# Kernel optimization log

Measured on AMD Instinct MI355X. Metric: run time of the kernel, lower is better.

The kernel has to match this reference:

```python
import jax, jax.numpy as jnp
import numpy as np

B, S, E, H = 2, 2048, 1024, 16
D = E // H  # head_dim = 64
EPS = 1e-6


def _angle_decay():
    # angle: 1/10000**linspace(0,1,D//2), each value repeated twice (interleaved)
    a = 1.0 / (10000.0 ** jnp.linspace(0.0, 1.0, D // 2))
    angle = jnp.repeat(a, 2)  # [D]
    decay = jnp.log(1.0 - 2.0 ** (-5.0 - jnp.arange(H, dtype=jnp.float32)))  # [H]
    return angle, decay


def _rel_pos(slen):
    angle, decay = _angle_decay()
    idx = jnp.arange(slen, dtype=jnp.float32)
    sin = jnp.sin(idx[:, None] * angle[None, :])  # [S, D]
    cos = jnp.cos(idx[:, None] * angle[None, :])  # [S, D]
    diff = idx[:, None] - idx[None, :]            # [S, S]
    tril = diff >= 0
    masked = jnp.where(tril, diff, jnp.inf)
    mask = jnp.exp(masked * decay[:, None, None])  # [H, S, S]; exp(-inf)=0 on upper tri
    mask = jnp.nan_to_num(mask)
    mask = mask / jnp.sqrt(jnp.sum(mask, axis=-1, keepdims=True))
    return sin, cos, mask


def _rotate_every_two(x):
    x1 = x[..., ::2]
    x2 = x[..., 1::2]
    return jnp.stack((-x2, x1), axis=-1).reshape(x.shape)


def _theta_shift(x, sin, cos):
    # x: [B, H, S, D]; sin/cos: [S, D] broadcast over B,H
    return x * cos + _rotate_every_two(x) * sin


def setup_inputs() -> dict:
    key = jax.random.key(0)
    ks = jax.random.split(key, 5)
    scale = 1.0 / np.sqrt(E)
    return {
        "x": jax.random.normal(ks[0], (B, S, E), dtype=jnp.float32),
        "Wq": jax.random.normal(ks[1], (E, E), dtype=jnp.float32) * scale,
        "Wk": jax.random.normal(ks[2], (E, E), dtype=jnp.float32) * scale,
        "Wv": jax.random.normal(ks[3], (E, E), dtype=jnp.float32) * scale,
        "Wg": jax.random.normal(ks[4], (E, E), dtype=jnp.float32) * scale,
    }


def reference(x, Wq, Wk, Wv, Wg):
    bsz, tgt_len, _ = x.shape
    sin, cos, mask = _rel_pos(tgt_len)
    scaling = E ** (-0.5)

    q = x @ Wq
    k = (x @ Wk) * scaling
    v = x @ Wv
    g = x @ Wg

    q = q.reshape(bsz, tgt_len, H, D).transpose(0, 2, 1, 3)  # [B,H,S,D]
    k = k.reshape(bsz, tgt_len, H, D).transpose(0, 2, 1, 3)
    vr = v.reshape(bsz, tgt_len, H, D).transpose(0, 2, 1, 3)

    qr = _theta_shift(q, sin, cos)
    kr = _theta_shift(k, sin, cos)

    qk = jnp.einsum("bhqd,bhkd->bhqk", qr, kr) * mask[None]
    denom = jax.lax.stop_gradient(
        jnp.clip(jnp.sum(jnp.abs(qk), axis=-1, keepdims=True), 1.0, 5e4)
    )
    out = jnp.einsum("bhqk,bhkd->bhqd", qk / denom, vr)
    out = out.transpose(0, 2, 1, 3)  # [B,S,H,D]

    # RMSNorm over head_dim (no affine)
    out = out * jax.lax.rsqrt(jnp.mean(out * out, axis=-1, keepdims=True) + EPS)
    out = out.reshape(bsz, tgt_len, E)
    return jax.nn.silu(g) * out
```

## Files before the change

kernel.cpp:

```cpp
#include <hip/hip_runtime.h>

typedef unsigned short u16;
typedef unsigned int u32;
typedef __attribute__((ext_vector_type(8))) __bf16 bf16x8;
typedef __attribute__((ext_vector_type(4))) float f32x4;

#define B_SZ   2
#define S_LEN  2048
#define E_DIM  1024
#define NHEAD  16
#define HD     64
#define KDIM   1024
#define NOUT   4096

__device__ __forceinline__ float bf2f(u16 u){
  union { u32 i; float f; } c; c.i = ((u32)u) << 16; return c.f;
}
__device__ __forceinline__ u16 f2bf(float f){
  union { float f; u32 i; } c; c.f = f;
  return (u16)((c.i + 0x7FFFu + ((c.i >> 16) & 1u)) >> 16);
}
__device__ __forceinline__ u16 f2bf_fast(float f){
  union { float f; u32 i; } c; c.f = f;
  return (u16)((c.i + 0x8000u) >> 16);
}
__device__ __forceinline__ void gl2lds16(const void* g, void* l){
  __builtin_amdgcn_global_load_lds((const __attribute__((address_space(1))) void*)g,
                                   (__attribute__((address_space(3))) void*)l, 16, 0, 0);
}

__global__ __launch_bounds__(256) void castx_kernel(const float* __restrict__ x, u16* __restrict__ xb){
  size_t flat = ((size_t)blockIdx.x * 256 + threadIdx.x) * 16;
  int m7 = (int)((flat >> 10) & 7);
  int cb = (int)((flat >> 3) & 7);
  size_t tile = flat & ~(size_t)63;
  float f[16];
  #pragma unroll
  for (int c = 0; c < 4; c++) *(float4*)&f[c * 4] = *(const float4*)&x[flat + c * 4];
  u16 o[16];
  #pragma unroll
  for (int i = 0; i < 16; i++) o[i] = f2bf(f[i]);
  *(uint4*)&xb[tile + ((cb ^ m7) * 8)]       = *(uint4*)&o[0];
  *(uint4*)&xb[tile + (((cb + 1) ^ m7) * 8)] = *(uint4*)&o[8];
}

__global__ __launch_bounds__(256) void wtrans_kernel(const float* __restrict__ Wq, const float* __restrict__ Wk,
                                                     const float* __restrict__ Wv, const float* __restrict__ Wg,
                                                     u16* __restrict__ WT){
  const float* Ws[4] = {Wq, Wk, Wv, Wg};
  const float* W = Ws[blockIdx.z];
  int n0 = blockIdx.x * 64, k0 = blockIdx.y * 64;
  __shared__ u16 tile[64][66];
  int t = threadIdx.x;
  int r = t >> 2, cg = (t & 3) * 16;
  const float* src = W + (size_t)(k0 + r) * E_DIM + n0 + cg;
  float f[16];
  #pragma unroll
  for (int c = 0; c < 4; c++) *(float4*)&f[c * 4] = *(const float4*)&src[c * 4];
  #pragma unroll
  for (int i = 0; i < 16; i++) tile[r][cg + i] = f2bf(f[i]);
  __syncthreads();
  u16 ov[16];
  #pragma unroll
  for (int i = 0; i < 16; i++) ov[i] = tile[cg + i][r];
  int n7 = r & 7, cb = cg >> 3;
  u16* dst = WT + (size_t)(blockIdx.z * E_DIM + n0 + r) * KDIM + k0;
  *(uint4*)&dst[(cb ^ n7) * 8]       = *(uint4*)&ov[0];
  *(uint4*)&dst[((cb + 1) ^ n7) * 8] = *(uint4*)&ov[8];
}

__global__ __launch_bounds__(256) void gemm_kernel(const u16* __restrict__ A, const u16* __restrict__ Bt,
                                                   u16* __restrict__ C){
  __shared__ __align__(16) u16 As[128 * 64];
  __shared__ __align__(16) u16 Bs[128 * 64];
  int m0 = blockIdx.y * 128, n0 = blockIdx.x * 128;
  int t = threadIdx.x;
  int wave = t >> 6, lane = t & 63;
  int l15 = lane & 15, quad = lane >> 4, h8 = lane & 7;
  int r0 = (wave & 1) * 64, c0 = (wave >> 1) * 64;
  f32x4 acc[4][4];
  #pragma unroll
  for (int i = 0; i < 4; i++)
    #pragma unroll
    for (int j = 0; j < 4; j++) acc[i][j] = (f32x4){0.f, 0.f, 0.f, 0.f};

  for (int k0 = 0; k0 < KDIM; k0 += 64){
    __syncthreads();
    #pragma unroll
    for (int c = 0; c < 4; c++){
      int L = c * 256 + t;
      gl2lds16(A + (size_t)(m0 + (L >> 3)) * KDIM + k0 + (L & 7) * 8, &As[L * 8]);
    }
    #pragma unroll
    for (int c = 0; c < 4; c++){
      int L = c * 256 + t;
      gl2lds16(Bt + (size_t)(n0 + (L >> 3)) * KDIM + k0 + (L & 7) * 8, &Bs[L * 8]);
    }
    __syncthreads();
    #pragma unroll
    for (int kk = 0; kk < 2; kk++){
      bf16x8 a[4], b[4];
      #pragma unroll
      for (int i = 0; i < 4; i++) a[i] = *(const bf16x8*)&As[(r0 + i * 16 + l15) * 64 + ((kk * 4 + quad) ^ h8) * 8];
      #pragma unroll
      for (int j = 0; j < 4; j++) b[j] = *(const bf16x8*)&Bs[(c0 + j * 16 + l15) * 64 + ((kk * 4 + quad) ^ h8) * 8];
      #pragma unroll
      for (int i = 0; i < 4; i++)
        #pragma unroll
        for (int j = 0; j < 4; j++)
          acc[i][j] = __builtin_amdgcn_mfma_f32_16x16x32_bf16(a[i], b[j], acc[i][j], 0, 0, 0);
    }
  }
  #pragma unroll
  for (int i = 0; i < 4; i++){
    int row = m0 + r0 + i * 16 + quad * 4;
    #pragma unroll
    for (int j = 0; j < 4; j++){
      int col = n0 + c0 + j * 16 + l15;
      #pragma unroll
      for (int r = 0; r < 4; r++)
        C[(size_t)(row + r) * NOUT + col] = f2bf(acc[i][j][r]);
    }
  }
}

__global__ __launch_bounds__(256) void shift_kernel(const u16* __restrict__ qkvg,
                                                    u16* __restrict__ qr, u16* __restrict__ kr,
                                                    u16* __restrict__ vt, u16* __restrict__ gc){
  int sb = blockIdx.x, bh = blockIdx.y;
  int s0 = sb * 64;
  int t = threadIdx.x;
  int sl = t >> 2, dg = (t & 3) * 16;
  int s = s0 + sl;
  int h = bh & 15;
  size_t token = (size_t)(bh >> 4) * S_LEN + s;
  size_t base = token * NOUT + h * HD + dg;
  u16 qv[16], kv[16], vv[16], gv[16];
  *(uint4*)&qv[0] = *(const uint4*)&qkvg[base];
  *(uint4*)&qv[8] = *(const uint4*)&qkvg[base + 8];
  *(uint4*)&kv[0] = *(const uint4*)&qkvg[base + 1024];
  *(uint4*)&kv[8] = *(const uint4*)&qkvg[base + 1024 + 8];
  *(uint4*)&vv[0] = *(const uint4*)&qkvg[base + 2048];
  *(uint4*)&vv[8] = *(const uint4*)&qkvg[base + 2048 + 8];
  *(uint4*)&gv[0] = *(const uint4*)&qkvg[base + 3072];
  *(uint4*)&gv[8] = *(const uint4*)&qkvg[base + 3072 + 8];
  size_t gdst = token * E_DIM + h * HD + dg;
  *(uint4*)&gc[gdst]     = *(uint4*)&gv[0];
  *(uint4*)&gc[gdst + 8] = *(uint4*)&gv[8];
  u16 qo[16], ko[16];
  #pragma unroll
  for (int i = 0; i < 8; i++){
    int dd = dg + 2 * i;
    float a = exp2f(-(float)(dd >> 1) * (13.287712379549449f / 31.0f));
    float ang = (float)s * a;
    float sn = sinf(ang), cs = cosf(ang);
    float qe = bf2f(qv[2 * i]), qd = bf2f(qv[2 * i + 1]);
    qo[2 * i]     = f2bf(qe * cs - qd * sn);
    qo[2 * i + 1] = f2bf(qd * cs + qe * sn);
    float ke = bf2f(kv[2 * i]) * 0.03125f, kd = bf2f(kv[2 * i + 1]) * 0.03125f;
    ko[2 * i]     = f2bf(ke * cs - kd * sn);
    ko[2 * i + 1] = f2bf(kd * cs + ke * sn);
  }
  size_t dsto = ((size_t)bh * S_LEN + s) * HD;
  *(uint4*)&qr[dsto + dg]     = *(uint4*)&qo[0];
  *(uint4*)&qr[dsto + dg + 8] = *(uint4*)&qo[8];
  int s7 = s & 7, cbk = dg >> 3;
  *(uint4*)&kr[dsto + ((cbk ^ s7) * 8)]       = *(uint4*)&ko[0];
  *(uint4*)&kr[dsto + (((cbk + 1) ^ s7) * 8)] = *(uint4*)&ko[8];
  __shared__ u16 vs[64][66];
  #pragma unroll
  for (int i = 0; i < 16; i++) vs[sl][dg + i] = vv[i];
  __syncthreads();
  int d = t >> 2, jg = (t & 3) * 16;
  u16 ov[16];
  #pragma unroll
  for (int i = 0; i < 16; i++) ov[i] = vs[jg + i][d];
  int d7 = d & 7, cbv = jg >> 3;
  size_t vrow = ((size_t)bh * HD + d) * S_LEN + s0;
  *(uint4*)&vt[vrow + ((cbv ^ d7) * 8)]       = *(uint4*)&ov[0];
  *(uint4*)&vt[vrow + (((cbv + 1) ^ d7) * 8)] = *(uint4*)&ov[8];
}

__global__ __launch_bounds__(256, 2) void retention_kernel(const u16* __restrict__ qr, const u16* __restrict__ kr,
                                                           const u16* __restrict__ vt,
                                                           float* __restrict__ pO, float* __restrict__ pBa){
  int bh = blockIdx.x;
  int qb = 15 - (int)blockIdx.y;
  int z  = blockIdx.z;
  int h = bh & 15;
  int q0 = qb * 128;
  __shared__ __align__(16) u16 Ks[64 * 64];
  __shared__ __align__(16) u16 Vs[64 * 64];
  __shared__ __align__(16) u16 Ps[128 * 72];
  int t = threadIdx.x, wave = t >> 6, lane = t & 63;
  int l15 = lane & 15, quad = lane >> 4, h8 = lane & 7;

  float decay = log1pf(-exp2f(-5.0f - (float)h));
  float negd = -decay;
  float estep = __expf(64.0f * negd);

  int qsE[2], rowb[2];
  #pragma unroll
  for (int e = 0; e < 2; e++){ rowb[e] = wave * 32 + e * 16; qsE[e] = q0 + rowb[e]; }

  bf16x8 qB[2][2];
  #pragma unroll
  for (int e = 0; e < 2; e++){
    size_t qrow = ((size_t)bh * S_LEN + qsE[e] + l15) * HD;
    qB[e][0] = *(const bf16x8*)&qr[qrow + quad * 8];
    qB[e][1] = *(const bf16x8*)&qr[qrow + 32 + quad * 8];
  }

  float win_f = 18.0f / negd;
  int win_i = (win_f > 2.1e9f) ? 0x7f000000 : (int)win_f;
  int z_lo = z ? (qb + 1) : 0;
  int z_hi = z ? (2 * qb + 1) : qb;
  int kb_lo = z_lo;
  {
    int jmin = q0 - win_i;
    if (jmin > z_lo * 64){ int wlo = jmin >> 6; kb_lo = wlo > z_lo ? wlo : z_lo; }
  }
  int k0s = kb_lo * 64;

  float em1d = expm1f(decay);
  float rfE[2]; int iE[2];
  #pragma unroll
  for (int e = 0; e < 2; e++){
    int i = qsE[e] + l15;
    iE[e] = i;
    float rowsum = expm1f((float)(i + 1) * decay) / em1d;
    rfE[e] = __expf((float)(i - k0s) * decay) * rsqrtf(rowsum);
  }
  float e1 = __expf(negd);
  float c16 = __expf(negd * 16.0f);
  float cbr[4];
  cbr[0] = __expf(negd * (float)(quad * 4));
  cbr[1] = cbr[0] * e1; cbr[2] = cbr[1] * e1; cbr[3] = cbr[2] * e1;

  f32x4 o[2][4];
  #pragma unroll
  for (int e = 0; e < 2; e++)
    #pragma unroll
    for (int dt = 0; dt < 4; dt++) o[e][dt] = (f32x4){0.f, 0.f, 0.f, 0.f};
  float babs[2] = {0.f, 0.f};

  const u16* krbh = kr + (size_t)bh * S_LEN * HD;
  const u16* vtbh = vt + (size_t)bh * HD * S_LEN;

  for (int kb = kb_lo; kb <= z_hi; kb++){
    int k0 = kb * 64;
    __syncthreads();
    #pragma unroll
    for (int c = 0; c < 2; c++){
      int L = c * 256 + t;
      gl2lds16(krbh + (size_t)k0 * HD + L * 8, &Ks[L * 8]);
    }
    #pragma unroll
    for (int c = 0; c < 2; c++){
      int L = c * 256 + t;
      gl2lds16(vtbh + (size_t)(L >> 3) * S_LEN + k0 + (L & 7) * 8, &Vs[L * 8]);
    }
    __syncthreads();

    bf16x8 kA0[4], kA1[4];
    #pragma unroll
    for (int ct = 0; ct < 4; ct++){
      int rw = (ct * 16 + l15) * 64;
      kA0[ct] = *(const bf16x8*)&Ks[rw + ((quad ^ h8) * 8)];
      kA1[ct] = *(const bf16x8*)&Ks[rw + (((quad + 4) ^ h8) * 8)];
    }
    #pragma unroll
    for (int e = 0; e < 2; e++){
      int qs = qsE[e];
      if (k0 <= qs + 15 && k0 + 63 >= qs - win_i){
        bool diag = (k0 + 64 > qs);
        float cf[4] = {cbr[0], cbr[1], cbr[2], cbr[3]};
        #pragma unroll
        for (int ct = 0; ct < 4; ct++){
          f32x4 zacc = (f32x4){0.f, 0.f, 0.f, 0.f};
          zacc = __builtin_amdgcn_mfma_f32_16x16x32_bf16(kA0[ct], qB[e][0], zacc, 0, 0, 0);
          zacc = __builtin_amdgcn_mfma_f32_16x16x32_bf16(kA1[ct], qB[e][1], zacc, 0, 0, 0);
          u16 pk[4];
          #pragma unroll
          for (int r = 0; r < 4; r++){
            float p = zacc[r] * (rfE[e] * cf[r]);
            if (diag && (k0 + ct * 16 + quad * 4 + r) > iE[e]) p = 0.f;
            babs[e] += fabsf(p);
            pk[r] = f2bf_fast(p);
            cf[r] *= c16;
          }
          u32 lo = (u32)pk[0] | ((u32)pk[1] << 16);
          u32 hi = (u32)pk[2] | ((u32)pk[3] << 16);
          *(uint2*)&Ps[(rowb[e] + l15) * 72 + ct * 16 + quad * 4] = make_uint2(lo, hi);
        }
      }
    }
    #pragma unroll
    for (int e = 0; e < 2; e++){
      int qs = qsE[e];
      if (k0 <= qs + 15 && k0 + 63 >= qs - win_i){
        bf16x8 pB0 = *(const bf16x8*)&Ps[(rowb[e] + l15) * 72 + quad * 8];
        bf16x8 pB1 = *(const bf16x8*)&Ps[(rowb[e] + l15) * 72 + 32 + quad * 8];
        #pragma unroll
        for (int dt = 0; dt < 4; dt++){
          int rw = (dt * 16 + l15) * 64;
          bf16x8 vA0 = *(const bf16x8*)&Vs[rw + ((quad ^ h8) * 8)];
          bf16x8 vA1 = *(const bf16x8*)&Vs[rw + (((quad + 4) ^ h8) * 8)];
          o[e][dt] = __builtin_amdgcn_mfma_f32_16x16x32_bf16(vA0, pB0, o[e][dt], 0, 0, 0);
          o[e][dt] = __builtin_amdgcn_mfma_f32_16x16x32_bf16(vA1, pB1, o[e][dt], 0, 0, 0);
        }
      }
    }
    #pragma unroll
    for (int e = 0; e < 2; e++) rfE[e] *= estep;
  }

  size_t slot = ((size_t)bh * 16 + qb) * 2 + z;
  float* po = pO + slot * (4 * 128 * 16);
  #pragma unroll
  for (int e = 0; e < 2; e++){
    float bsum = babs[e];
    bsum += __shfl_xor(bsum, 16);
    bsum += __shfl_xor(bsum, 32);
    if (quad == 0) pBa[slot * 128 + rowb[e] + l15] = bsum;
    #pragma unroll
    for (int dt = 0; dt < 4; dt++)
      *(float4*)&po[(dt * 128 + rowb[e] + l15) * 16 + quad * 4] = *(float4*)&o[e][dt];
  }
}

__global__ __launch_bounds__(128) void combine_kernel(const float* __restrict__ pO, const float* __restrict__ pBa,
                                                      const u16* __restrict__ gc, float* __restrict__ out){
  int bh = blockIdx.x, qb = blockIdx.y;
  int b = bh >> 4, h = bh & 15;
  int i = threadIdx.x;
  int s = qb * 128 + i;
  size_t s2 = ((size_t)bh * 16 + qb) * 2;
  const float* p0 = pO + s2 * 8192;
  const float* p1 = p0 + 8192;
  float v[64];
  #pragma unroll
  for (int dt = 0; dt < 4; dt++)
    #pragma unroll
    for (int c = 0; c < 4; c++){
      float4 a  = *(const float4*)&p0[(dt * 128 + i) * 16 + c * 4];
      float4 bb = *(const float4*)&p1[(dt * 128 + i) * 16 + c * 4];
      int d = dt * 16 + c * 4;
      v[d + 0] = a.x + bb.x; v[d + 1] = a.y + bb.y;
      v[d + 2] = a.z + bb.z; v[d + 3] = a.w + bb.w;
    }
  float bsum = pBa[s2 * 128 + i] + pBa[(s2 + 1) * 128 + i];
  float dinv = 1.0f / fminf(fmaxf(bsum, 1.0f), 50000.0f);
  float ssq = 0.f;
  #pragma unroll
  for (int d = 0; d < 64; d++){ v[d] *= dinv; ssq += v[d] * v[d]; }
  float rms = rsqrtf(ssq * (1.0f / 64.0f) + 1e-6f);
  size_t gbase = ((size_t)b * S_LEN + s) * E_DIM + h * HD;
  u16 gu[64];
  #pragma unroll
  for (int c = 0; c < 8; c++) *(uint4*)&gu[c * 8] = *(const uint4*)&gc[gbase + c * 8];
  float ov[64];
  #pragma unroll
  for (int d = 0; d < 64; d++){
    float gv = bf2f(gu[d]);
    float sg = gv / (1.0f + __expf(-gv));
    ov[d] = v[d] * rms * sg;
  }
  float* obase = out + ((size_t)b * S_LEN + s) * E_DIM + h * HD;
  #pragma unroll
  for (int c = 0; c < 16; c++) *(float4*)&obase[c * 4] = *(float4*)&ov[c * 4];
}

extern "C" void kernel_launch(void* const* d_in, const int* in_sizes, int n_in,
                              void* d_out, int out_size, void* d_ws, size_t ws_size,
                              hipStream_t stream){
  const float* x  = (const float*)d_in[0];
  const float* Wq = (const float*)d_in[1];
  const float* Wk = (const float*)d_in[2];
  const float* Wv = (const float*)d_in[3];
  const float* Wg = (const float*)d_in[4];
  float* out = (float*)d_out;
  char* ws = (char*)d_ws;
  u16*   xb   = (u16*)(ws);
  u16*   WT   = (u16*)(ws + (8ull  << 20));
  u16*   qkvg = (u16*)(ws + (16ull << 20));
  u16*   qrp  = (u16*)(ws);
  u16*   vtp  = (u16*)(ws + (8ull  << 20));
  float* pO   = (float*)(ws + (16ull << 20));
  u16*   krp  = (u16*)(ws + (48ull << 20));
  u16*   gcp  = (u16*)(ws + (56ull << 20));
  float* pBa  = (float*)(ws + (64ull << 20));

  castx_kernel    <<<dim3(1024),       256, 0, stream>>>(x, xb);
  wtrans_kernel   <<<dim3(16, 16, 4),  256, 0, stream>>>(Wq, Wk, Wv, Wg, WT);
  gemm_kernel     <<<dim3(32, 32),     256, 0, stream>>>(xb, WT, qkvg);
  shift_kernel    <<<dim3(32, 32),     256, 0, stream>>>(qkvg, qrp, krp, vtp, gcp);
  retention_kernel<<<dim3(32, 16, 2),  256, 0, stream>>>(qrp, krp, vtp, pO, pBa);
  combine_kernel  <<<dim3(32, 16),     128, 0, stream>>>(pO, pBa, gcp, out);
}
```

Before: 195.1 us.

## Fuse rotary shift, V transpose and gate copy into GEMM epilogue

```diff
diff --git a/kernel.cpp b/kernel.cpp
--- a/kernel.cpp
+++ b/kernel.cpp
@@ -70,9 +70,11 @@
 }
 
 __global__ __launch_bounds__(256) void gemm_kernel(const u16* __restrict__ A, const u16* __restrict__ Bt,
-                                                   u16* __restrict__ C){
-  __shared__ __align__(16) u16 As[128 * 64];
-  __shared__ __align__(16) u16 Bs[128 * 64];
+                                                   u16* __restrict__ qr, u16* __restrict__ kr,
+                                                   u16* __restrict__ vt, u16* __restrict__ gc){
+  __shared__ __align__(16) u16 smem[17408];
+  u16* As = smem;
+  u16* Bs = smem + 8192;
   int m0 = blockIdx.y * 128, n0 = blockIdx.x * 128;
   int t = threadIdx.x;
   int wave = t >> 6, lane = t & 63;
@@ -111,74 +113,84 @@
           acc[i][j] = __builtin_amdgcn_mfma_f32_16x16x32_bf16(a[i], b[j], acc[i][j], 0, 0, 0);
     }
   }
-  #pragma unroll
-  for (int i = 0; i < 4; i++){
-    int row = m0 + r0 + i * 16 + quad * 4;
+
+  int zone = n0 >> 10;
+  int b = m0 >> 11;
+  int sbase = (m0 & 2047) + r0;
+
+  if (zone == 3){
+    int ebase = (n0 & 1023) + c0;
+    #pragma unroll
+    for (int i = 0; i < 4; i++){
+      int tok = m0 + r0 + i * 16 + quad * 4;
+      #pragma unroll
+      for (int j = 0; j < 4; j++){
+        int e = ebase + j * 16 + l15;
+        #pragma unroll
+        for (int r = 0; r < 4; r++)
+          gc[(size_t)(tok + r) * E_DIM + e] = f2bf(acc[i][j][r]);
+      }
+    }
+  } else if (zone == 2){
+    __syncthreads();
+    u16* Tw = smem + wave * 4352;
+    #pragma unroll
+    for (int i = 0; i < 4; i++)
+      #pragma unroll
+      for (int j = 0; j < 4; j++){
+        int d = j * 16 + l15;
+        u16 pk[4];
+        #pragma unroll
+        for (int r = 0; r < 4; r++) pk[r] = f2bf(acc[i][j][r]);
+        *(uint2*)&Tw[d * 68 + i * 16 + quad * 4] = *(uint2*)pk;
+      }
+    __syncthreads();
+    int h = ((n0 & 1023) >> 6) + (c0 >> 6);
+    size_t bh = (size_t)b * 16 + h;
+    int sgq = lane >> 4;
+    #pragma unroll
+    for (int it = 0; it < 4; it++){
+      int dd = (lane & 15) + 16 * it;
+      u16 ov[16];
+      *(uint4*)&ov[0] = *(const uint4*)&Tw[dd * 68 + sgq * 16];
+      *(uint4*)&ov[8] = *(const uint4*)&Tw[dd * 68 + sgq * 16 + 8];
+      int s0 = sbase + sgq * 16;
+      int d7 = dd & 7;
+      int cb = (s0 & 63) >> 3;
+      size_t vrow = (bh * HD + dd) * S_LEN + (s0 & ~63);
+      *(uint4*)&vt[vrow + ((cb ^ d7) * 8)]       = *(uint4*)&ov[0];
+      *(uint4*)&vt[vrow + (((cb + 1) ^ d7) * 8)] = *(uint4*)&ov[8];
+    }
+  } else {
+    float scale = (zone == 1) ? 0.03125f : 1.0f;
+    int h = ((n0 & 1023) >> 6) + (c0 >> 6);
+    size_t bh = (size_t)b * 16 + h;
+    float sgn = (l15 & 1) ? 1.0f : -1.0f;
     #pragma unroll
     for (int j = 0; j < 4; j++){
-      int col = n0 + c0 + j * 16 + l15;
-      #pragma unroll
-      for (int r = 0; r < 4; r++)
-        C[(size_t)(row + r) * NOUT + col] = f2bf(acc[i][j][r]);
-    }
-  }
-}
-
-__global__ __launch_bounds__(256) void shift_kernel(const u16* __restrict__ qkvg,
-                                                    u16* __restrict__ qr, u16* __restrict__ kr,
-                                                    u16* __restrict__ vt, u16* __restrict__ gc){
-  int sb = blockIdx.x, bh = blockIdx.y;
-  int s0 = sb * 64;
-  int t = threadIdx.x;
-  int sl = t >> 2, dg = (t & 3) * 16;
-  int s = s0 + sl;
-  int h = bh & 15;
-  size_t token = (size_t)(bh >> 4) * S_LEN + s;
-  size_t base = token * NOUT + h * HD + dg;
-  u16 qv[16], kv[16], vv[16], gv[16];
-  *(uint4*)&qv[0] = *(const uint4*)&qkvg[base];
-  *(uint4*)&qv[8] = *(const uint4*)&qkvg[base + 8];
-  *(uint4*)&kv[0] = *(const uint4*)&qkvg[base + 1024];
-  *(uint4*)&kv[8] = *(const uint4*)&qkvg[base + 1024 + 8];
-  *(uint4*)&vv[0] = *(const uint4*)&qkvg[base + 2048];
-  *(uint4*)&vv[8] = *(const uint4*)&qkvg[base + 2048 + 8];
-  *(uint4*)&gv[0] = *(const uint4*)&qkvg[base + 3072];
-  *(uint4*)&gv[8] = *(const uint4*)&qkvg[base + 3072 + 8];
-  size_t gdst = token * E_DIM + h * HD + dg;
-  *(uint4*)&gc[gdst]     = *(uint4*)&gv[0];
-  *(uint4*)&gc[gdst + 8] = *(uint4*)&gv[8];
-  u16 qo[16], ko[16];
-  #pragma unroll
-  for (int i = 0; i < 8; i++){
-    int dd = dg + 2 * i;
-    float a = exp2f(-(float)(dd >> 1) * (13.287712379549449f / 31.0f));
-    float ang = (float)s * a;
-    float sn = sinf(ang), cs = cosf(ang);
-    float qe = bf2f(qv[2 * i]), qd = bf2f(qv[2 * i + 1]);
-    qo[2 * i]     = f2bf(qe * cs - qd * sn);
-    qo[2 * i + 1] = f2bf(qd * cs + qe * sn);
-    float ke = bf2f(kv[2 * i]) * 0.03125f, kd = bf2f(kv[2 * i + 1]) * 0.03125f;
-    ko[2 * i]     = f2bf(ke * cs - kd * sn);
-    ko[2 * i + 1] = f2bf(kd * cs + ke * sn);
-  }
-  size_t dsto = ((size_t)bh * S_LEN + s) * HD;
-  *(uint4*)&qr[dsto + dg]     = *(uint4*)&qo[0];
-  *(uint4*)&qr[dsto + dg + 8] = *(uint4*)&qo[8];
-  int s7 = s & 7, cbk = dg >> 3;
-  *(uint4*)&kr[dsto + ((cbk ^ s7) * 8)]       = *(uint4*)&ko[0];
-  *(uint4*)&kr[dsto + (((cbk + 1) ^ s7) * 8)] = *(uint4*)&ko[8];
-  __shared__ u16 vs[64][66];
-  #pragma unroll
-  for (int i = 0; i < 16; i++) vs[sl][dg + i] = vv[i];
-  __syncthreads();
-  int d = t >> 2, jg = (t & 3) * 16;
-  u16 ov[16];
-  #pragma unroll
-  for (int i = 0; i < 16; i++) ov[i] = vs[jg + i][d];
-  int d7 = d & 7, cbv = jg >> 3;
-  size_t vrow = ((size_t)bh * HD + d) * S_LEN + s0;
-  *(uint4*)&vt[vrow + ((cbv ^ d7) * 8)]       = *(uint4*)&ov[0];
-  *(uint4*)&vt[vrow + (((cbv + 1) ^ d7) * 8)] = *(uint4*)&ov[8];
+      int d = j * 16 + l15;
+      float a = exp2f(-(float)(d >> 1) * (13.287712379549449f / 31.0f));
+      #pragma unroll
+      for (int i = 0; i < 4; i++){
+        #pragma unroll
+        for (int r = 0; r < 4; r++){
+          int s = sbase + i * 16 + quad * 4 + r;
+          float v = acc[i][j][r] * scale;
+          float p = __shfl_xor(v, 1);
+          float ang = (float)s * a;
+          float sn = __sinf(ang), cs = __cosf(ang);
+          float rv = fmaf(sgn * p, sn, v * cs);
+          size_t base = (bh * S_LEN + s) * HD;
+          if (zone == 0){
+            qr[base + d] = f2bf(rv);
+          } else {
+            int cb = d >> 3, s7 = s & 7;
+            kr[base + ((cb ^ s7) * 8) + (d & 7)] = f2bf(rv);
+          }
+        }
+      }
+    }
+  }
 }
 
 __global__ __launch_bounds__(256, 2) void retention_kernel(const u16* __restrict__ qr, const u16* __restrict__ kr,
@@ -381,20 +393,18 @@
   const float* Wg = (const float*)d_in[4];
   float* out = (float*)d_out;
   char* ws = (char*)d_ws;
-  u16*   xb   = (u16*)(ws);
-  u16*   WT   = (u16*)(ws + (8ull  << 20));
-  u16*   qkvg = (u16*)(ws + (16ull << 20));
-  u16*   qrp  = (u16*)(ws);
-  u16*   vtp  = (u16*)(ws + (8ull  << 20));
-  float* pO   = (float*)(ws + (16ull << 20));
-  u16*   krp  = (u16*)(ws + (48ull << 20));
-  u16*   gcp  = (u16*)(ws + (56ull << 20));
-  float* pBa  = (float*)(ws + (64ull << 20));
+  u16*   xb  = (u16*)(ws);
+  u16*   WT  = (u16*)(ws + (8ull  << 20));
+  float* pO  = (float*)(ws);
+  u16*   qrp = (u16*)(ws + (32ull << 20));
+  u16*   krp = (u16*)(ws + (40ull << 20));
+  u16*   vtp = (u16*)(ws + (48ull << 20));
+  u16*   gcp = (u16*)(ws + (56ull << 20));
+  float* pBa = (float*)(ws + (64ull << 20));
 
   castx_kernel    <<<dim3(1024),       256, 0, stream>>>(x, xb);
   wtrans_kernel   <<<dim3(16, 16, 4),  256, 0, stream>>>(Wq, Wk, Wv, Wg, WT);
-  gemm_kernel     <<<dim3(32, 32),     256, 0, stream>>>(xb, WT, qkvg);
-  shift_kernel    <<<dim3(32, 32),     256, 0, stream>>>(qkvg, qrp, krp, vtp, gcp);
+  gemm_kernel     <<<dim3(32, 32),     256, 0, stream>>>(xb, WT, qrp, krp, vtp, gcp);
   retention_kernel<<<dim3(32, 16, 2),  256, 0, stream>>>(qrp, krp, vtp, pO, pBa);
   combine_kernel  <<<dim3(32, 16),     128, 0, stream>>>(pO, pBa, gcp, out);
 }
```

Result: slower. 232.5 us (+19.2%).

## Write gate directly from GEMM, store partial outputs in bf16, shrink decay window

Applied to the files above, without the earlier changes.

```diff
diff --git a/kernel.cpp b/kernel.cpp
--- a/kernel.cpp
+++ b/kernel.cpp
@@ -11,7 +11,7 @@
 #define NHEAD  16
 #define HD     64
 #define KDIM   1024
-#define NOUT   4096
+#define NQKV   3072
 
 __device__ __forceinline__ float bf2f(u16 u){
   union { u32 i; float f; } c; c.i = ((u32)u) << 16; return c.f;
@@ -70,7 +70,7 @@
 }
 
 __global__ __launch_bounds__(256) void gemm_kernel(const u16* __restrict__ A, const u16* __restrict__ Bt,
-                                                   u16* __restrict__ C){
+                                                   u16* __restrict__ qkv, u16* __restrict__ gc){
   __shared__ __align__(16) u16 As[128 * 64];
   __shared__ __align__(16) u16 Bs[128 * 64];
   int m0 = blockIdx.y * 128, n0 = blockIdx.x * 128;
@@ -111,22 +111,36 @@
           acc[i][j] = __builtin_amdgcn_mfma_f32_16x16x32_bf16(a[i], b[j], acc[i][j], 0, 0, 0);
     }
   }
-  #pragma unroll
-  for (int i = 0; i < 4; i++){
-    int row = m0 + r0 + i * 16 + quad * 4;
-    #pragma unroll
-    for (int j = 0; j < 4; j++){
-      int col = n0 + c0 + j * 16 + l15;
-      #pragma unroll
-      for (int r = 0; r < 4; r++)
-        C[(size_t)(row + r) * NOUT + col] = f2bf(acc[i][j][r]);
-    }
-  }
-}
-
-__global__ __launch_bounds__(256) void shift_kernel(const u16* __restrict__ qkvg,
+  if (n0 < 3072){
+    #pragma unroll
+    for (int i = 0; i < 4; i++){
+      int row = m0 + r0 + i * 16 + quad * 4;
+      #pragma unroll
+      for (int j = 0; j < 4; j++){
+        int col = n0 + c0 + j * 16 + l15;
+        #pragma unroll
+        for (int r = 0; r < 4; r++)
+          qkv[(size_t)(row + r) * NQKV + col] = f2bf(acc[i][j][r]);
+      }
+    }
+  } else {
+    #pragma unroll
+    for (int i = 0; i < 4; i++){
+      int row = m0 + r0 + i * 16 + quad * 4;
+      #pragma unroll
+      for (int j = 0; j < 4; j++){
+        int e = (n0 - 3072) + c0 + j * 16 + l15;
+        #pragma unroll
+        for (int r = 0; r < 4; r++)
+          gc[(size_t)(row + r) * E_DIM + e] = f2bf(acc[i][j][r]);
+      }
+    }
+  }
+}
+
+__global__ __launch_bounds__(256) void shift_kernel(const u16* __restrict__ qkv,
                                                     u16* __restrict__ qr, u16* __restrict__ kr,
-                                                    u16* __restrict__ vt, u16* __restrict__ gc){
+                                                    u16* __restrict__ vt){
   int sb = blockIdx.x, bh = blockIdx.y;
   int s0 = sb * 64;
   int t = threadIdx.x;
@@ -134,19 +148,14 @@
   int s = s0 + sl;
   int h = bh & 15;
   size_t token = (size_t)(bh >> 4) * S_LEN + s;
-  size_t base = token * NOUT + h * HD + dg;
-  u16 qv[16], kv[16], vv[16], gv[16];
-  *(uint4*)&qv[0] = *(const uint4*)&qkvg[base];
-  *(uint4*)&qv[8] = *(const uint4*)&qkvg[base + 8];
-  *(uint4*)&kv[0] = *(const uint4*)&qkvg[base + 1024];
-  *(uint4*)&kv[8] = *(const uint4*)&qkvg[base + 1024 + 8];
-  *(uint4*)&vv[0] = *(const uint4*)&qkvg[base + 2048];
-  *(uint4*)&vv[8] = *(const uint4*)&qkvg[base + 2048 + 8];
-  *(uint4*)&gv[0] = *(const uint4*)&qkvg[base + 3072];
-  *(uint4*)&gv[8] = *(const uint4*)&qkvg[base + 3072 + 8];
-  size_t gdst = token * E_DIM + h * HD + dg;
-  *(uint4*)&gc[gdst]     = *(uint4*)&gv[0];
-  *(uint4*)&gc[gdst + 8] = *(uint4*)&gv[8];
+  size_t base = token * NQKV + h * HD + dg;
+  u16 qv[16], kv[16], vv[16];
+  *(uint4*)&qv[0] = *(const uint4*)&qkv[base];
+  *(uint4*)&qv[8] = *(const uint4*)&qkv[base + 8];
+  *(uint4*)&kv[0] = *(const uint4*)&qkv[base + 1024];
+  *(uint4*)&kv[8] = *(const uint4*)&qkv[base + 1024 + 8];
+  *(uint4*)&vv[0] = *(const uint4*)&qkv[base + 2048];
+  *(uint4*)&vv[8] = *(const uint4*)&qkv[base + 2048 + 8];
   u16 qo[16], ko[16];
   #pragma unroll
   for (int i = 0; i < 8; i++){
@@ -183,7 +192,7 @@
 
 __global__ __launch_bounds__(256, 2) void retention_kernel(const u16* __restrict__ qr, const u16* __restrict__ kr,
                                                            const u16* __restrict__ vt,
-                                                           float* __restrict__ pO, float* __restrict__ pBa){
+                                                           u16* __restrict__ pO, float* __restrict__ pBa){
   int bh = blockIdx.x;
   int qb = 15 - (int)blockIdx.y;
   int z  = blockIdx.z;
@@ -211,7 +220,7 @@
     qB[e][1] = *(const bf16x8*)&qr[qrow + 32 + quad * 8];
   }
 
-  float win_f = 18.0f / negd;
+  float win_f = 11.0f / negd;
   int win_i = (win_f > 2.1e9f) ? 0x7f000000 : (int)win_f;
   int z_lo = z ? (qb + 1) : 0;
   int z_hi = z ? (2 * qb + 1) : qb;
@@ -316,7 +325,7 @@
   }
 
   size_t slot = ((size_t)bh * 16 + qb) * 2 + z;
-  float* po = pO + slot * (4 * 128 * 16);
+  u16* po = pO + slot * (4 * 128 * 16);
   #pragma unroll
   for (int e = 0; e < 2; e++){
     float bsum = babs[e];
@@ -324,31 +333,35 @@
     bsum += __shfl_xor(bsum, 32);
     if (quad == 0) pBa[slot * 128 + rowb[e] + l15] = bsum;
     #pragma unroll
-    for (int dt = 0; dt < 4; dt++)
-      *(float4*)&po[(dt * 128 + rowb[e] + l15) * 16 + quad * 4] = *(float4*)&o[e][dt];
-  }
-}
-
-__global__ __launch_bounds__(128) void combine_kernel(const float* __restrict__ pO, const float* __restrict__ pBa,
+    for (int dt = 0; dt < 4; dt++){
+      u16 pk[4];
+      #pragma unroll
+      for (int r = 0; r < 4; r++) pk[r] = f2bf(o[e][dt][r]);
+      *(uint2*)&po[(dt * 128 + rowb[e] + l15) * 16 + quad * 4] = *(uint2*)pk;
+    }
+  }
+}
+
+__global__ __launch_bounds__(128) void combine_kernel(const u16* __restrict__ pO, const float* __restrict__ pBa,
                                                       const u16* __restrict__ gc, float* __restrict__ out){
   int bh = blockIdx.x, qb = blockIdx.y;
   int b = bh >> 4, h = bh & 15;
   int i = threadIdx.x;
   int s = qb * 128 + i;
   size_t s2 = ((size_t)bh * 16 + qb) * 2;
-  const float* p0 = pO + s2 * 8192;
-  const float* p1 = p0 + 8192;
+  const u16* p0 = pO + s2 * 8192;
+  const u16* p1 = p0 + 8192;
   float v[64];
   #pragma unroll
-  for (int dt = 0; dt < 4; dt++)
-    #pragma unroll
-    for (int c = 0; c < 4; c++){
-      float4 a  = *(const float4*)&p0[(dt * 128 + i) * 16 + c * 4];
-      float4 bb = *(const float4*)&p1[(dt * 128 + i) * 16 + c * 4];
-      int d = dt * 16 + c * 4;
-      v[d + 0] = a.x + bb.x; v[d + 1] = a.y + bb.y;
-      v[d + 2] = a.z + bb.z; v[d + 3] = a.w + bb.w;
-    }
+  for (int dt = 0; dt < 4; dt++){
+    u16 a[16], bb[16];
+    *(uint4*)&a[0]  = *(const uint4*)&p0[(dt * 128 + i) * 16];
+    *(uint4*)&a[8]  = *(const uint4*)&p0[(dt * 128 + i) * 16 + 8];
+    *(uint4*)&bb[0] = *(const uint4*)&p1[(dt * 128 + i) * 16];
+    *(uint4*)&bb[8] = *(const uint4*)&p1[(dt * 128 + i) * 16 + 8];
+    #pragma unroll
+    for (int c = 0; c < 16; c++) v[dt * 16 + c] = bf2f(a[c]) + bf2f(bb[c]);
+  }
   float bsum = pBa[s2 * 128 + i] + pBa[(s2 + 1) * 128 + i];
   float dinv = 1.0f / fminf(fmaxf(bsum, 1.0f), 50000.0f);
   float ssq = 0.f;
@@ -381,20 +394,20 @@
   const float* Wg = (const float*)d_in[4];
   float* out = (float*)d_out;
   char* ws = (char*)d_ws;
-  u16*   xb   = (u16*)(ws);
-  u16*   WT   = (u16*)(ws + (8ull  << 20));
-  u16*   qkvg = (u16*)(ws + (16ull << 20));
-  u16*   qrp  = (u16*)(ws);
-  u16*   vtp  = (u16*)(ws + (8ull  << 20));
-  float* pO   = (float*)(ws + (16ull << 20));
-  u16*   krp  = (u16*)(ws + (48ull << 20));
-  u16*   gcp  = (u16*)(ws + (56ull << 20));
-  float* pBa  = (float*)(ws + (64ull << 20));
+  u16*   xb  = (u16*)(ws);
+  u16*   WT  = (u16*)(ws + (8ull  << 20));
+  u16*   qkv = (u16*)(ws + (16ull << 20));
+  u16*   gcp = (u16*)(ws + (40ull << 20));
+  u16*   vtp = (u16*)(ws);
+  u16*   qrp = (u16*)(ws + (8ull  << 20));
+  u16*   pO  = (u16*)(ws + (16ull << 20));
+  u16*   krp = (u16*)(ws + (48ull << 20));
+  float* pBa = (float*)(ws + (56ull << 20));
 
   castx_kernel    <<<dim3(1024),       256, 0, stream>>>(x, xb);
   wtrans_kernel   <<<dim3(16, 16, 4),  256, 0, stream>>>(Wq, Wk, Wv, Wg, WT);
-  gemm_kernel     <<<dim3(32, 32),     256, 0, stream>>>(xb, WT, qkvg);
-  shift_kernel    <<<dim3(32, 32),     256, 0, stream>>>(qkvg, qrp, krp, vtp, gcp);
+  gemm_kernel     <<<dim3(32, 32),     256, 0, stream>>>(xb, WT, qkv, gcp);
+  shift_kernel    <<<dim3(32, 32),     256, 0, stream>>>(qkv, qrp, krp, vtp);
   retention_kernel<<<dim3(32, 16, 2),  256, 0, stream>>>(qrp, krp, vtp, pO, pBa);
   combine_kernel  <<<dim3(32, 16),     128, 0, stream>>>(pO, pBa, gcp, out);
 }
```

Result: no change. 192.6 us (-1.3%).
